# Optimization experiments

Hardware: AMD Instinct MI355X
Metric: run time of the kernel (lower is better)

The kernel has to match this reference:

```python
import jax, jax.numpy as jnp
import numpy as np

B, C, H, W = 4, 256, 64, 64

def setup_inputs() -> dict:
    key = jax.random.key(0)
    ks = jax.random.split(key, 6)
    inv = 1.0 / np.sqrt(C)
    return {
        "feature": jax.random.normal(ks[0], (B, C, H, W), dtype=jnp.float32),
        "flow": jax.random.normal(ks[1], (B, 2, H, W), dtype=jnp.float32),
        "q_w": jax.random.uniform(ks[2], (C, C), dtype=jnp.float32, minval=-inv, maxval=inv),
        "q_b": jax.random.uniform(ks[3], (C,), dtype=jnp.float32, minval=-inv, maxval=inv),
        "k_w": jax.random.uniform(ks[4], (C, C), dtype=jnp.float32, minval=-inv, maxval=inv),
        "k_b": jax.random.uniform(ks[5], (C,), dtype=jnp.float32, minval=-inv, maxval=inv),
    }

def reference(feature, flow, q_w, q_b, k_w, k_b):
    b, c, h, w = feature.shape
    # [b,c,h,w] -> [b, h*w, c] tokens
    tok = feature.reshape(b, c, h * w).transpose(0, 2, 1)
    v = flow.reshape(b, 2, h * w).transpose(0, 2, 1)       # [b, hw, 2]
    q = jnp.einsum('bnc,dc->bnd', tok, q_w) + q_b           # Linear(c,c)
    k = jnp.einsum('bnc,dc->bnd', tok, k_w) + k_b
    scale = 1.0 / jnp.sqrt(jnp.asarray(c, dtype=q.dtype))
    scores = jnp.einsum('bld,bsd->bls', q, k) * scale       # [b, hw, hw]
    attn = jax.nn.softmax(scores, axis=-1)                  # dropout_p=0 -> no-op
    out = jnp.einsum('bls,bsv->blv', attn, v)               # [b, hw, 2]
    return out.reshape(b, h, w, 2).transpose(0, 3, 1, 2)    # [b, 2, h, w]
```

## Files before the change

kernel.cpp:

```cpp
#include <hip/hip_runtime.h>
#include <math.h>

#define BB 4
#define CC 256
#define HWN 4096
#define NTOK 16384
#define SCQ 0.09016844136f

typedef __attribute__((ext_vector_type(8))) short short8;
typedef __attribute__((ext_vector_type(4))) float f32x4;
typedef unsigned short ushort_t;

__device__ __forceinline__ ushort_t f2bf(float f) {
    unsigned int u = __float_as_uint(f);
    unsigned int r = (u + 0x7FFFu + ((u >> 16) & 1u)) >> 16;
    return (ushort_t)r;
}
__device__ __forceinline__ unsigned int pack2(float a, float b) {
    return (unsigned int)f2bf(a) | ((unsigned int)f2bf(b) << 16);
}
__device__ __forceinline__ float fexp2(float x) {
#if __has_builtin(__builtin_amdgcn_exp2f)
    return __builtin_amdgcn_exp2f(x);
#else
    return exp2f(x);
#endif
}

__global__ __launch_bounds__(256) void prep_kernel(
    const float* __restrict__ feature,
    const float* __restrict__ q_w, const float* __restrict__ k_w,
    ushort_t* __restrict__ fbuf,
    ushort_t* __restrict__ qwb, ushort_t* __restrict__ kwb,
    float* __restrict__ zbuf)
{
    int bid = blockIdx.x;
    int tid = threadIdx.x;

    if (bid >= 1024) {
        int t = (bid - 1024) * 256 + tid;
        float4 q4 = *(const float4*)&q_w[(size_t)t * 4];
        float4 k4 = *(const float4*)&k_w[(size_t)t * 4];
        unsigned long long qo = (unsigned long long)pack2(q4.x * SCQ, q4.y * SCQ)
                              | ((unsigned long long)pack2(q4.z * SCQ, q4.w * SCQ) << 32);
        unsigned long long ko = (unsigned long long)pack2(k4.x, k4.y)
                              | ((unsigned long long)pack2(k4.z, k4.w) << 32);
        *(unsigned long long*)&qwb[(size_t)t * 4] = qo;
        *(unsigned long long*)&kwb[(size_t)t * 4] = ko;
        zbuf[t] = 0.f; zbuf[t + NTOK] = 0.f; zbuf[t + 2 * NTOK] = 0.f;
        return;
    }

    int b   = bid >> 8;
    int rem = bid & 255;
    int cch = rem >> 6;
    int nch = rem & 63;

    __shared__ float lsA[64][69];

    int cl = tid >> 2, tg = (tid & 3) * 16;
    const float* src = feature + (size_t)(b * CC + cch * 64 + cl) * HWN + nch * 64 + tg;
    *(float4*)&lsA[cl][tg]      = *(const float4*)(src);
    *(float4*)&lsA[cl][tg + 4]  = *(const float4*)(src + 4);
    *(float4*)&lsA[cl][tg + 8]  = *(const float4*)(src + 8);
    *(float4*)&lsA[cl][tg + 12] = *(const float4*)(src + 12);
    __syncthreads();

    int tokw = tid >> 2, c16 = (tid & 3) * 16;
    unsigned int u[8];
    #pragma unroll
    for (int j = 0; j < 8; j++)
        u[j] = pack2(lsA[c16 + 2 * j][tokw], lsA[c16 + 2 * j + 1][tokw]);
    size_t orow = (size_t)(b * HWN + nch * 64 + tokw) * CC + cch * 64 + c16;
    *(uint4*)&fbuf[orow]     = *(uint4*)&u[0];
    *(uint4*)&fbuf[orow + 8] = *(uint4*)&u[4];
}

__global__ __launch_bounds__(256, 2) void proj_kernel(
    const ushort_t* __restrict__ fbuf,
    const ushort_t* __restrict__ qwb, const ushort_t* __restrict__ kwb,
    const float* __restrict__ q_bias, const float* __restrict__ k_bias,
    ushort_t* __restrict__ qb, ushort_t* __restrict__ kb)
{
    int id = blockIdx.x;
    int dh = id >> 8;
    int inner = id & 255;
    int b   = inner & 3;
    int tch = inner >> 2;
    int tok0 = tch * 64;

    int t = threadIdx.x, w = t >> 6, lane = t & 63;
    int n16 = lane & 15, quad = lane >> 4;

    int d0 = dh * 64 + w * 16;

    short8 aq[8], ak[8];
    #pragma unroll
    for (int kc = 0; kc < 8; kc++) {
        size_t off = (size_t)(d0 + n16) * CC + kc * 32 + quad * 8;
        aq[kc] = *(const short8*)&qwb[off];
        ak[kc] = *(const short8*)&kwb[off];
    }
    float bqv[4], bkv[4];
    #pragma unroll
    for (int r = 0; r < 4; r++) {
        bqv[r] = q_bias[d0 + quad * 4 + r] * SCQ;
        bkv[r] = k_bias[d0 + quad * 4 + r];
    }

    int kcq   = d0 >> 5;
    int quadA = ((d0 >> 4) & 1) * 2 + (quad >> 1);
    int halfo = quad & 1;

    #pragma unroll
    for (int tokt = 0; tokt < 4; tokt++) {
        size_t trow = (size_t)(b * HWN + tok0 + tokt * 16 + n16) * CC;
        short8 bf[8];
        #pragma unroll
        for (int kc = 0; kc < 8; kc++)
            bf[kc] = *(const short8*)&fbuf[trow + kc * 32 + quad * 8];
        f32x4 accq = (f32x4){0.f, 0.f, 0.f, 0.f};
        f32x4 acck = (f32x4){0.f, 0.f, 0.f, 0.f};
        #pragma unroll
        for (int kc = 0; kc < 8; kc++) {
            accq = __builtin_amdgcn_mfma_f32_16x16x32_bf16(aq[kc], bf[kc], accq, 0, 0, 0);
            acck = __builtin_amdgcn_mfma_f32_16x16x32_bf16(ak[kc], bf[kc], acck, 0, 0, 0);
        }
        ushort4 oq, ok;
        oq.x = f2bf(accq[0] + bqv[0]); oq.y = f2bf(accq[1] + bqv[1]);
        oq.z = f2bf(accq[2] + bqv[2]); oq.w = f2bf(accq[3] + bqv[3]);
        ok.x = f2bf(acck[0] + bkv[0]); ok.y = f2bf(acck[1] + bkv[1]);
        ok.z = f2bf(acck[2] + bkv[2]); ok.w = f2bf(acck[3] + bkv[3]);
        int tt_tile = tch * 4 + tokt;
        size_t gbyte = (((size_t)(b * 256 + tt_tile) * 512) + kcq * 64 + quadA * 16 + n16) * 16
                       + halfo * 8;
        *(ushort4*)((char*)qb + gbyte) = oq;
        *(ushort4*)((char*)kb + gbyte) = ok;
    }
}

__global__ __launch_bounds__(256, 2) void attn_kernel(
    const ushort_t* __restrict__ qb, const ushort_t* __restrict__ kb,
    const float* __restrict__ flow,
    float* __restrict__ den_g, float* __restrict__ nx_g, float* __restrict__ ny_g)
{
    int id = (blockIdx.x & 7) * 128 + (blockIdx.x >> 3);
    int qt = id & 63; id >>= 6;
    int sr = id & 3;  id >>= 2;
    int b = id;

    int t = threadIdx.x;
    int w = t >> 6, lane = t & 63;
    int n16 = lane & 15, quad = lane >> 4;

    int q0 = qt * 64;
    int s_beg = sr * 1024;

    __shared__ __align__(16) ushort_t qlds[16384];
    __shared__ float lflow[2048];

    const float* fx = flow + (size_t)b * 2 * HWN;
    const float* fy = fx + HWN;
    #pragma unroll
    for (int i = 0; i < 4; i++) {
        lflow[t + i * 256]        = fx[s_beg + t + i * 256];
        lflow[1024 + t + i * 256] = fy[s_beg + t + i * 256];
    }

    {
        const char* qsrc = (const char*)qb + ((size_t)(b * 256 + (q0 >> 4)) * 512) * 16;
        char* qdst = (char*)qlds;
        #pragma unroll
        for (int i = 0; i < 8; i++)
            __builtin_amdgcn_global_load_lds(
                (const __attribute__((address_space(1))) unsigned int*)(qsrc + (i * 256 + t) * 16),
                (__attribute__((address_space(3))) unsigned int*)(qdst + (i * 256 + t) * 16),
                16, 0, 0);
    }
    __syncthreads();

    const char* kbase = (const char*)kb
        + ((size_t)(b * 256 + (s_beg >> 4) + w * 16) * 512 + lane) * 16;
    const char* qldsb = (const char*)qlds + (size_t)lane * 16;

    float den[4], nxa[4], nya[4];
    #pragma unroll
    for (int i = 0; i < 4; i++) { den[i] = 0.f; nxa[i] = 0.f; nya[i] = 0.f; }

    for (int round = 0; round < 8; round++) {
        short8 kf0[8], kf1[8];
        #pragma unroll
        for (int kc = 0; kc < 8; kc++) {
            kf0[kc] = *(const short8*)(kbase + (round * 2 + 0) * 8192 + kc * 1024);
            kf1[kc] = *(const short8*)(kbase + (round * 2 + 1) * 8192 + kc * 1024);
        }
        int klbase = w * 256 + round * 32 + quad * 4;
        f32x4 vx0 = *(const f32x4*)&lflow[klbase];
        f32x4 vx1 = *(const f32x4*)&lflow[klbase + 16];
        f32x4 vy0 = *(const f32x4*)&lflow[1024 + klbase];
        f32x4 vy1 = *(const f32x4*)&lflow[1024 + klbase + 16];

        #pragma unroll
        for (int qtl = 0; qtl < 4; qtl++) {
            f32x4 a0 = (f32x4){0.f, 0.f, 0.f, 0.f};
            f32x4 a1 = (f32x4){0.f, 0.f, 0.f, 0.f};
            #pragma unroll
            for (int kc = 0; kc < 8; kc++) {
                short8 qf = *(const short8*)(qldsb + qtl * 8192 + kc * 1024);
                a0 = __builtin_amdgcn_mfma_f32_16x16x32_bf16(kf0[kc], qf, a0, 0, 0, 0);
                a1 = __builtin_amdgcn_mfma_f32_16x16x32_bf16(kf1[kc], qf, a1, 0, 0, 0);
            }
            float d_ = 0.f, x_ = 0.f, y_ = 0.f;
            #pragma unroll
            for (int r = 0; r < 4; r++) {
                float p0 = fexp2(a0[r]);
                float p1 = fexp2(a1[r]);
                d_ += p0 + p1;
                x_ = fmaf(p0, vx0[r], x_); x_ = fmaf(p1, vx1[r], x_);
                y_ = fmaf(p0, vy0[r], y_); y_ = fmaf(p1, vy1[r], y_);
            }
            den[qtl] += d_; nxa[qtl] += x_; nya[qtl] += y_;
        }
    }

    #pragma unroll
    for (int qtl = 0; qtl < 4; qtl++) {
        float dv = den[qtl], xv = nxa[qtl], yv = nya[qtl];
        dv += __shfl_down(dv, 32); dv += __shfl_down(dv, 16);
        xv += __shfl_down(xv, 32); xv += __shfl_down(xv, 16);
        yv += __shfl_down(yv, 32); yv += __shfl_down(yv, 16);
        if (lane < 16) {
            int qrow = q0 + qtl * 16 + n16;
            int gi = b * HWN + qrow;
            atomicAdd(&den_g[gi], dv);
            atomicAdd(&nx_g[gi],  xv);
            atomicAdd(&ny_g[gi],  yv);
        }
    }
}

__global__ __launch_bounds__(256) void finalize_kernel(
    const float* __restrict__ den_g, const float* __restrict__ nx_g,
    const float* __restrict__ ny_g, float* __restrict__ out)
{
    int idx = blockIdx.x * 256 + threadIdx.x;
    int b = idx >> 12, n = idx & 4095;
    float inv = 1.0f / den_g[idx];
    out[(size_t)b * 2 * HWN + n]       = nx_g[idx] * inv;
    out[(size_t)b * 2 * HWN + HWN + n] = ny_g[idx] * inv;
}

extern "C" void kernel_launch(void* const* d_in, const int* in_sizes, int n_in,
                              void* d_out, int out_size, void* d_ws, size_t ws_size,
                              hipStream_t stream) {
    const float* feature = (const float*)d_in[0];
    const float* flow    = (const float*)d_in[1];
    const float* q_w     = (const float*)d_in[2];
    const float* q_b     = (const float*)d_in[3];
    const float* k_w     = (const float*)d_in[4];
    const float* k_b     = (const float*)d_in[5];
    float* out = (float*)d_out;

    ushort_t* qbuf = (ushort_t*)d_ws;
    ushort_t* kbuf = qbuf + (size_t)NTOK * CC;
    float* den = (float*)(kbuf + (size_t)NTOK * CC);
    float* nx  = den + NTOK;
    float* ny  = nx + NTOK;
    ushort_t* qwb = (ushort_t*)(ny + NTOK);
    ushort_t* kwb = qwb + (size_t)CC * CC;
    ushort_t* fbuf = kwb + (size_t)CC * CC;

    prep_kernel<<<1088, 256, 0, stream>>>(feature, q_w, k_w, fbuf, qwb, kwb, den);
    proj_kernel<<<1024, 256, 0, stream>>>(fbuf, qwb, kwb, q_b, k_b, qbuf, kbuf);
    attn_kernel<<<1024, 256, 0, stream>>>(qbuf, kbuf, flow, den, nx, ny);
    finalize_kernel<<<64, 256, 0, stream>>>(den, nx, ny, out);
}
```

Measured before the change: 143.4 us.

## Fuse feature transpose into projection kernel via shared-memory staging

After: 131.5 us. 1.09x faster.

```diff
diff --git a/kernel.cpp b/kernel.cpp
--- a/kernel.cpp
+++ b/kernel.cpp
@@ -27,115 +27,105 @@
 #endif
 }
 
-__global__ __launch_bounds__(256) void prep_kernel(
-    const float* __restrict__ feature,
+__global__ __launch_bounds__(256) void wprep_kernel(
     const float* __restrict__ q_w, const float* __restrict__ k_w,
-    ushort_t* __restrict__ fbuf,
     ushort_t* __restrict__ qwb, ushort_t* __restrict__ kwb,
     float* __restrict__ zbuf)
 {
-    int bid = blockIdx.x;
-    int tid = threadIdx.x;
-
-    if (bid >= 1024) {
-        int t = (bid - 1024) * 256 + tid;
-        float4 q4 = *(const float4*)&q_w[(size_t)t * 4];
-        float4 k4 = *(const float4*)&k_w[(size_t)t * 4];
-        unsigned long long qo = (unsigned long long)pack2(q4.x * SCQ, q4.y * SCQ)
-                              | ((unsigned long long)pack2(q4.z * SCQ, q4.w * SCQ) << 32);
-        unsigned long long ko = (unsigned long long)pack2(k4.x, k4.y)
-                              | ((unsigned long long)pack2(k4.z, k4.w) << 32);
-        *(unsigned long long*)&qwb[(size_t)t * 4] = qo;
-        *(unsigned long long*)&kwb[(size_t)t * 4] = ko;
-        zbuf[t] = 0.f; zbuf[t + NTOK] = 0.f; zbuf[t + 2 * NTOK] = 0.f;
-        return;
-    }
-
-    int b   = bid >> 8;
-    int rem = bid & 255;
-    int cch = rem >> 6;
-    int nch = rem & 63;
-
-    __shared__ float lsA[64][69];
-
-    int cl = tid >> 2, tg = (tid & 3) * 16;
-    const float* src = feature + (size_t)(b * CC + cch * 64 + cl) * HWN + nch * 64 + tg;
-    *(float4*)&lsA[cl][tg]      = *(const float4*)(src);
-    *(float4*)&lsA[cl][tg + 4]  = *(const float4*)(src + 4);
-    *(float4*)&lsA[cl][tg + 8]  = *(const float4*)(src + 8);
-    *(float4*)&lsA[cl][tg + 12] = *(const float4*)(src + 12);
-    __syncthreads();
-
-    int tokw = tid >> 2, c16 = (tid & 3) * 16;
-    unsigned int u[8];
-    #pragma unroll
-    for (int j = 0; j < 8; j++)
-        u[j] = pack2(lsA[c16 + 2 * j][tokw], lsA[c16 + 2 * j + 1][tokw]);
-    size_t orow = (size_t)(b * HWN + nch * 64 + tokw) * CC + cch * 64 + c16;
-    *(uint4*)&fbuf[orow]     = *(uint4*)&u[0];
-    *(uint4*)&fbuf[orow + 8] = *(uint4*)&u[4];
+    int t = blockIdx.x * 256 + threadIdx.x;
+    float4 q4 = *(const float4*)&q_w[(size_t)t * 4];
+    float4 k4 = *(const float4*)&k_w[(size_t)t * 4];
+    unsigned long long qo = (unsigned long long)pack2(q4.x * SCQ, q4.y * SCQ)
+                          | ((unsigned long long)pack2(q4.z * SCQ, q4.w * SCQ) << 32);
+    unsigned long long ko = (unsigned long long)pack2(k4.x, k4.y)
+                          | ((unsigned long long)pack2(k4.z, k4.w) << 32);
+    *(unsigned long long*)&qwb[(size_t)t * 4] = qo;
+    *(unsigned long long*)&kwb[(size_t)t * 4] = ko;
+    zbuf[t] = 0.f; zbuf[t + NTOK] = 0.f; zbuf[t + 2 * NTOK] = 0.f;
 }
 
 __global__ __launch_bounds__(256, 2) void proj_kernel(
-    const ushort_t* __restrict__ fbuf,
+    const float* __restrict__ feature,
     const ushort_t* __restrict__ qwb, const ushort_t* __restrict__ kwb,
     const float* __restrict__ q_bias, const float* __restrict__ k_bias,
     ushort_t* __restrict__ qb, ushort_t* __restrict__ kb)
 {
     int id = blockIdx.x;
     int dh = id >> 8;
-    int inner = id & 255;
-    int b   = inner & 3;
-    int tch = inner >> 2;
-    int tok0 = tch * 64;
+    id &= 255;
+    int tt = id & 63;
+    int b  = id >> 6;
+    int tok0 = tt * 64;
 
     int t = threadIdx.x, w = t >> 6, lane = t & 63;
     int n16 = lane & 15, quad = lane >> 4;
 
-    int d0 = dh * 64 + w * 16;
-
-    short8 aq[8], ak[8];
-    #pragma unroll
-    for (int kc = 0; kc < 8; kc++) {
-        size_t off = (size_t)(d0 + n16) * CC + kc * 32 + quad * 8;
-        aq[kc] = *(const short8*)&qwb[off];
-        ak[kc] = *(const short8*)&kwb[off];
-    }
-    float bqv[4], bkv[4];
-    #pragma unroll
-    for (int r = 0; r < 4; r++) {
-        bqv[r] = q_bias[d0 + quad * 4 + r] * SCQ;
-        bkv[r] = k_bias[d0 + quad * 4 + r];
-    }
-
-    int kcq   = d0 >> 5;
-    int quadA = ((d0 >> 4) & 1) * 2 + (quad >> 1);
-    int halfo = quad & 1;
-
-    #pragma unroll
-    for (int tokt = 0; tokt < 4; tokt++) {
-        size_t trow = (size_t)(b * HWN + tok0 + tokt * 16 + n16) * CC;
-        short8 bf[8];
-        #pragma unroll
-        for (int kc = 0; kc < 8; kc++)
-            bf[kc] = *(const short8*)&fbuf[trow + kc * 32 + quad * 8];
-        f32x4 accq = (f32x4){0.f, 0.f, 0.f, 0.f};
-        f32x4 acck = (f32x4){0.f, 0.f, 0.f, 0.f};
+    __shared__ float    lsA[64][69];
+    __shared__ ushort_t lsB[64][264];
+
+    const float* F = feature + (size_t)(b * CC) * HWN;
+
+    int cl = t >> 2, tg = (t & 3) * 16;
+    int tokw = t >> 2, c16 = (t & 3) * 16;
+
+    for (int ch = 0; ch < 4; ch++) {
+        const float* src = F + (size_t)(ch * 64 + cl) * HWN + tok0 + tg;
+        *(float4*)&lsA[cl][tg]      = *(const float4*)(src);
+        *(float4*)&lsA[cl][tg + 4]  = *(const float4*)(src + 4);
+        *(float4*)&lsA[cl][tg + 8]  = *(const float4*)(src + 8);
+        *(float4*)&lsA[cl][tg + 12] = *(const float4*)(src + 12);
+        __syncthreads();
+        #pragma unroll
+        for (int jj = 0; jj < 8; jj++)
+            *(unsigned int*)&lsB[tokw][ch * 64 + c16 + 2 * jj] =
+                pack2(lsA[c16 + 2 * jj][tokw], lsA[c16 + 2 * jj + 1][tokw]);
+        __syncthreads();
+    }
+
+    int dw0 = dh * 128 + w * 32;
+    #pragma unroll
+    for (int dsub = 0; dsub < 2; dsub++) {
+        int d0 = dw0 + dsub * 16;
+        f32x4 accq[4], acck[4];
+        #pragma unroll
+        for (int i = 0; i < 4; i++) {
+            accq[i] = (f32x4){0.f, 0.f, 0.f, 0.f};
+            acck[i] = (f32x4){0.f, 0.f, 0.f, 0.f};
+        }
         #pragma unroll
         for (int kc = 0; kc < 8; kc++) {
-            accq = __builtin_amdgcn_mfma_f32_16x16x32_bf16(aq[kc], bf[kc], accq, 0, 0, 0);
-            acck = __builtin_amdgcn_mfma_f32_16x16x32_bf16(ak[kc], bf[kc], acck, 0, 0, 0);
-        }
-        ushort4 oq, ok;
-        oq.x = f2bf(accq[0] + bqv[0]); oq.y = f2bf(accq[1] + bqv[1]);
-        oq.z = f2bf(accq[2] + bqv[2]); oq.w = f2bf(accq[3] + bqv[3]);
-        ok.x = f2bf(acck[0] + bkv[0]); ok.y = f2bf(acck[1] + bkv[1]);
-        ok.z = f2bf(acck[2] + bkv[2]); ok.w = f2bf(acck[3] + bkv[3]);
-        int tt_tile = tch * 4 + tokt;
-        size_t gbyte = (((size_t)(b * 256 + tt_tile) * 512) + kcq * 64 + quadA * 16 + n16) * 16
-                       + halfo * 8;
-        *(ushort4*)((char*)qb + gbyte) = oq;
-        *(ushort4*)((char*)kb + gbyte) = ok;
+            size_t off = (size_t)(d0 + n16) * CC + kc * 32 + quad * 8;
+            short8 aq = *(const short8*)&qwb[off];
+            short8 ak = *(const short8*)&kwb[off];
+            #pragma unroll
+            for (int tokt = 0; tokt < 4; tokt++) {
+                short8 bf = *(const short8*)&lsB[tokt * 16 + n16][kc * 32 + quad * 8];
+                accq[tokt] = __builtin_amdgcn_mfma_f32_16x16x32_bf16(aq, bf, accq[tokt], 0, 0, 0);
+                acck[tokt] = __builtin_amdgcn_mfma_f32_16x16x32_bf16(ak, bf, acck[tokt], 0, 0, 0);
+            }
+        }
+        float bqv[4], bkv[4];
+        #pragma unroll
+        for (int r = 0; r < 4; r++) {
+            bqv[r] = q_bias[d0 + quad * 4 + r] * SCQ;
+            bkv[r] = k_bias[d0 + quad * 4 + r];
+        }
+        int kcq   = d0 >> 5;
+        int quadA = ((d0 >> 4) & 1) * 2 + (quad >> 1);
+        int halfo = quad & 1;
+        #pragma unroll
+        for (int tokt = 0; tokt < 4; tokt++) {
+            ushort4 oq, ok;
+            oq.x = f2bf(accq[tokt][0] + bqv[0]); oq.y = f2bf(accq[tokt][1] + bqv[1]);
+            oq.z = f2bf(accq[tokt][2] + bqv[2]); oq.w = f2bf(accq[tokt][3] + bqv[3]);
+            ok.x = f2bf(acck[tokt][0] + bkv[0]); ok.y = f2bf(acck[tokt][1] + bkv[1]);
+            ok.z = f2bf(acck[tokt][2] + bkv[2]); ok.w = f2bf(acck[tokt][3] + bkv[3]);
+            int tt_tile = tt * 4 + tokt;
+            size_t gbyte = (((size_t)(b * 256 + tt_tile) * 512) + kcq * 64 + quadA * 16 + n16) * 16
+                           + halfo * 8;
+            *(ushort4*)((char*)qb + gbyte) = oq;
+            *(ushort4*)((char*)kb + gbyte) = ok;
+        }
     }
 }
 
@@ -268,10 +258,9 @@
     float* ny  = nx + NTOK;
     ushort_t* qwb = (ushort_t*)(ny + NTOK);
     ushort_t* kwb = qwb + (size_t)CC * CC;
-    ushort_t* fbuf = kwb + (size_t)CC * CC;
-
-    prep_kernel<<<1088, 256, 0, stream>>>(feature, q_w, k_w, fbuf, qwb, kwb, den);
-    proj_kernel<<<1024, 256, 0, stream>>>(fbuf, qwb, kwb, q_b, k_b, qbuf, kbuf);
+
+    wprep_kernel<<<64, 256, 0, stream>>>(q_w, k_w, qwb, kwb, den);
+    proj_kernel<<<512, 256, 0, stream>>>(feature, qwb, kwb, q_b, k_b, qbuf, kbuf);
     attn_kernel<<<1024, 256, 0, stream>>>(qbuf, kbuf, flow, den, nx, ny);
     finalize_kernel<<<64, 256, 0, stream>>>(den, nx, ny, out);
 }
```
